# Optimization experiments

Measured on AMD Instinct MI355X. Metric: run time of the kernel, lower is better.

## Reference

```python
import jax, jax.numpy as jnp
import numpy as np

N = 100_000   # nodes
E = 1_600_000 # edges (avg degree 16)
D0, D1, D2 = 128, 64, 64


def _linp(key, n_out, n_in):
    kw, kb = jax.random.split(key)
    s = 1.0 / np.sqrt(n_in)
    W = jax.random.uniform(kw, (n_out, n_in), jnp.float32, -s, s)
    b = jax.random.uniform(kb, (n_out,), jnp.float32, -s, s)
    return W, b


def setup_inputs() -> dict:
    key = jax.random.key(0)
    ks = jax.random.split(key, 9)
    h = jax.random.normal(ks[0], (N, D0), jnp.float32)
    # guarantee every row has at least one edge (avoids empty-row softmax / 0-std NaNs)
    rows = jnp.concatenate([jnp.arange(N, dtype=jnp.int32),
                            jax.random.randint(ks[1], (E - N,), 0, N, jnp.int32)])
    cols = jax.random.randint(ks[2], (E,), 0, N, jnp.int32)
    edge_index = jnp.stack([rows, cols])  # [2, E], row = softmax segment
    W11, b11 = _linp(ks[3], D1, D0)
    W12, b12 = _linp(ks[4], 1, D1)
    W13, b13 = _linp(ks[5], D1, D0)
    W21, b21 = _linp(ks[6], D2, D1)
    W22, b22 = _linp(ks[7], 1, D2)
    W23, b23 = _linp(ks[8], D2, D1)
    return dict(h=h, edge_index=edge_index,
                W11=W11, b11=b11, W12=W12, b12=b12, W13=W13, b13=b13,
                W21=W21, b21=b21, W22=W22, b22=b22, W23=W23, b23=b23)


def reference(h, edge_index, W11, b11, W12, b12, W13, b13,
              W21, b21, W22, b22, W23, b23):
    src, dst = edge_index[0], edge_index[1]

    def gat_layer(x, Wa, ba, We, be, Wv, bv):
        a = jnp.tanh(x @ Wa.T + ba)                       # [N, d] node scores (l11/l21)
        e = jnp.tanh((a[src] + a[dst]) @ We.T + be)[:, 0] # [E] per-edge logit (l12/l22)
        # per-row (segment) softmax over src = row index
        m = jax.ops.segment_max(e, src, num_segments=N)
        ex = jnp.exp(e - m[src])
        denom = jax.ops.segment_sum(ex, src, num_segments=N)
        att = ex / denom[src]                             # [E]
        v = jnp.tanh(x @ Wv.T + bv)                       # [N, d] values (l13/l23)
        out = jax.ops.segment_sum(att[:, None] * v[dst], src, num_segments=N)  # sparse mm
        return out / jnp.std(out, -1, keepdims=True, ddof=1)  # torch.std is unbiased

    h = gat_layer(h, W11, b11, W12, b12, W13, b13)
    h = gat_layer(h, W21, b21, W22, b22, W23, b23)
    return h
```

## Files before the change

### kernel.cpp

```cpp
#include <hip/hip_runtime.h>


#define WS_ALIGN 256
#define BIN_SHIFT 7
#define BIN_NODES 128
#define BIN_CAP 2560
#define MAX_BINS 1024
#define EPB 4096

typedef __attribute__((ext_vector_type(8))) short short8;
typedef __attribute__((ext_vector_type(4))) float f32x4;

__device__ __forceinline__ float wave_sum(float x) {
#pragma unroll
  for (int m = 32; m > 0; m >>= 1) x += __shfl_xor(x, m, 64);
  return x;
}

__device__ __forceinline__ float fast_tanh(float x) {
  x = fminf(15.f, fmaxf(-15.f, x));
  float e = __expf(2.f * x);
  return (e - 1.f) * __builtin_amdgcn_rcpf(e + 1.f);
}

__device__ __forceinline__ void prepw_one(const float* __restrict__ Wa,
                                          const float* __restrict__ Wv,
                                          short* __restrict__ Wh, short* __restrict__ Wl,
                                          int K, int i) {
  int KBLK = K / 32;
  int j = i & 7;
  int c = (i >> 3) & 15;
  int q = (i >> 7) & 3;
  int r = i >> 9;
  int nt = r / KBLK, kb = r - nt * KBLK;
  int row = nt * 16 + c;
  int col = kb * 32 + q * 8 + j;
  float f = (row < 64) ? Wa[row * K + col] : Wv[(row - 64) * K + col];
  unsigned u = __float_as_uint(f);
  float hf = __uint_as_float(u & 0xffff0000u);
  Wh[i] = (short)(u >> 16);
  Wl[i] = (short)(__float_as_uint(f - hf) >> 16);
}

__global__ void k_setup(const float* __restrict__ W11, const float* __restrict__ W13,
                        short* __restrict__ Wh1, short* __restrict__ Wl1,
                        const float* __restrict__ W21, const float* __restrict__ W23,
                        short* __restrict__ Wh2, short* __restrict__ Wl2,
                        int* __restrict__ cursor, int nb) {
  int i = blockIdx.x * 256 + threadIdx.x;
  if (i < 16384) {
    prepw_one(W11, W13, Wh1, Wl1, 128, i);
  } else if (i < 16384 + 8192) {
    prepw_one(W21, W23, Wh2, Wl2, 64, i - 16384);
  } else {
    int b = i - 24576;
    if (b < nb) cursor[b] = b * BIN_CAP;
  }
}

__global__ __launch_bounds__(256) void k_bin(const int* __restrict__ src,
                                             const int* __restrict__ dst,
                                             int* __restrict__ cursor,
                                             int* __restrict__ binned, int E, int nb) {
  __shared__ int ssrc[EPB];
  __shared__ int sdst[EPB];
  __shared__ int hist[MAX_BINS];
  __shared__ int base[MAX_BINS];
  int t = threadIdx.x;
  for (int i = t; i < nb; i += 256) hist[i] = 0;
  __syncthreads();
  int e0 = blockIdx.x * EPB;
  for (int i = t; i < EPB; i += 256) {
    int e = e0 + i;
    int sv = -1, dv = 0;
    if (e < E) {
      sv = src[e];
      dv = dst[e];
      atomicAdd(&hist[sv >> BIN_SHIFT], 1);
    }
    ssrc[i] = sv;
    sdst[i] = dv;
  }
  __syncthreads();
  for (int b = t; b < nb; b += 256) {
    int c = hist[b];
    base[b] = c ? atomicAdd(&cursor[b], c) : 0;
    hist[b] = 0;
  }
  __syncthreads();
  for (int i = t; i < EPB; i += 256) {
    int sv = ssrc[i];
    if (sv >= 0) {
      int b = sv >> BIN_SHIFT;
      int r = atomicAdd(&hist[b], 1);
      int pos = base[b] + r;
      if (pos < (b + 1) * BIN_CAP)
        binned[pos] = (sdst[i] << BIN_SHIFT) | (sv & (BIN_NODES - 1));
    }
  }
}

__global__ __launch_bounds__(256) void k_sort_bin(int* __restrict__ binned,
                                                  const int* __restrict__ cursor,
                                                  int* __restrict__ rs,
                                                  int* __restrict__ re, int n) {
  __shared__ int ents[BIN_CAP];
  __shared__ int sorted[BIN_CAP];
  __shared__ int hist[BIN_NODES];
  __shared__ int scan[BIN_NODES];
  __shared__ int cur[BIN_NODES];
  int bin = blockIdx.x;
  int t = threadIdx.x;
  int nbase = bin << BIN_SHIFT;
  int cnt = cursor[bin] - bin * BIN_CAP;
  if (cnt > BIN_CAP) cnt = BIN_CAP;
  if (t < BIN_NODES) hist[t] = 0;
  __syncthreads();
  int* bp = binned + (size_t)bin * BIN_CAP;
  for (int i = t; i < cnt; i += 256) {
    int pk = bp[i];
    ents[i] = pk;
    atomicAdd(&hist[pk & (BIN_NODES - 1)], 1);
  }
  __syncthreads();
  if (t < BIN_NODES) scan[t] = hist[t];
  __syncthreads();
  for (int off = 1; off < BIN_NODES; off <<= 1) {
    int add = (t < BIN_NODES && t >= off) ? scan[t - off] : 0;
    __syncthreads();
    if (t < BIN_NODES) scan[t] += add;
    __syncthreads();
  }
  if (t < BIN_NODES) {
    int ex = scan[t] - hist[t];
    cur[t] = ex;
    int node = nbase + t;
    if (node < n) {
      rs[node] = bin * BIN_CAP + ex;
      re[node] = bin * BIN_CAP + ex + hist[t];
    }
  }
  __syncthreads();
  for (int i = t; i < cnt; i += 256) {
    int pk = ents[i];
    int pos = atomicAdd(&cur[pk & (BIN_NODES - 1)], 1);
    sorted[pos] = pk;
  }
  __syncthreads();
  for (int i = t; i < cnt; i += 256) {
    int pk = sorted[i];
    int node = pk & (BIN_NODES - 1);
    int hi = scan[node];
    int lo = hi - hist[node];
    int r = lo;
    for (int j = lo; j < hi; j++) {
      int pj = sorted[j];
      r += (pj < pk) || (pj == pk && j < i);
    }
    ents[r] = pk >> BIN_SHIFT;
  }
  __syncthreads();
  for (int i = t; i < cnt; i += 256) bp[i] = ents[i];
}

template <int K>
__global__ __launch_bounds__(256) void k_node(
    const float* __restrict__ x, const short* __restrict__ Wh,
    const short* __restrict__ Wl, const float* __restrict__ ba,
    const float* __restrict__ we, const float* __restrict__ bv,
    float* __restrict__ v_out, float* __restrict__ s_out, int n) {
  constexpr int KBLK = K / 32;
  constexpr int KP = K + 4;
  __shared__ float sx[64 * KP];
  int t = threadIdx.x;
  int l = t & 63;
  int w = t >> 6;
  int q = l >> 4, c = l & 15;
  int node0b = blockIdx.x * 64;

  {
    const float4* xg = (const float4*)(x + (size_t)node0b * K);
    constexpr int R4 = K / 4;
#pragma unroll
    for (int it = 0; it < 64 * R4 / 256; it++) {
      int i = it * 256 + t;
      int r = i / R4, k4 = i - r * R4;
      float4 val = (node0b + r < n) ? xg[i] : (float4){0.f, 0.f, 0.f, 0.f};
      *(float4*)&sx[r * KP + k4 * 4] = val;
    }
  }
  __syncthreads();

  int node0w = node0b + w * 16;
  if (node0w >= n) return;

  const short8* WhF = (const short8*)Wh;
  const short8* WlF = (const short8*)Wl;

  f32x4 acc[8];
#pragma unroll
  for (int i = 0; i < 8; i++) acc[i] = (f32x4){0.f, 0.f, 0.f, 0.f};

  const float* xl = sx + (w * 16 + c) * KP;

#pragma unroll 1
  for (int kb = 0; kb < KBLK; kb++) {
    float4 x0 = *(const float4*)&xl[kb * 32 + q * 8];
    float4 x1 = *(const float4*)&xl[kb * 32 + q * 8 + 4];
    float xv[8] = {x0.x, x0.y, x0.z, x0.w, x1.x, x1.y, x1.z, x1.w};
    short8 ah, al;
#pragma unroll
    for (int j = 0; j < 8; j++) {
      unsigned u = __float_as_uint(xv[j]);
      ah[j] = (short)(u >> 16);
      float hf = __uint_as_float(u & 0xffff0000u);
      al[j] = (short)(__float_as_uint(xv[j] - hf) >> 16);
    }
#pragma unroll
    for (int nt = 0; nt < 8; nt++) {
      short8 wh = WhF[(size_t)(nt * KBLK + kb) * 64 + l];
      short8 wl = WlF[(size_t)(nt * KBLK + kb) * 64 + l];
      acc[nt] = __builtin_amdgcn_mfma_f32_16x16x32_bf16(ah, wh, acc[nt], 0, 0, 0);
      acc[nt] = __builtin_amdgcn_mfma_f32_16x16x32_bf16(ah, wl, acc[nt], 0, 0, 0);
      acc[nt] = __builtin_amdgcn_mfma_f32_16x16x32_bf16(al, wh, acc[nt], 0, 0, 0);
    }
  }

  float p[4] = {0.f, 0.f, 0.f, 0.f};
#pragma unroll
  for (int nt = 0; nt < 4; nt++) {
    int o = nt * 16 + c;
    float bav = ba[o], wev = we[o];
#pragma unroll
    for (int r = 0; r < 4; r++) p[r] += fast_tanh(acc[nt][r] + bav) * wev;
  }
#pragma unroll
  for (int mm = 1; mm < 16; mm <<= 1) {
#pragma unroll
    for (int r = 0; r < 4; r++) p[r] += __shfl_xor(p[r], mm, 64);
  }
  if (c == 0) {
#pragma unroll
    for (int r = 0; r < 4; r++) {
      int node = node0w + q * 4 + r;
      if (node < n) s_out[node] = p[r];
    }
  }
#pragma unroll
  for (int nt = 4; nt < 8; nt++) {
    int o = (nt - 4) * 16 + c;
    float bvv = bv[o];
#pragma unroll
    for (int r = 0; r < 4; r++) {
      int node = node0w + q * 4 + r;
      if (node < n)
        v_out[(size_t)node * 64 + o] = fast_tanh(acc[nt][r] + bvv);
    }
  }
}

__global__ __launch_bounds__(256) void k_aggr(const int* __restrict__ rs,
                                              const int* __restrict__ re,
                                              const int* __restrict__ col,
                                              const float* __restrict__ s,
                                              const float* __restrict__ be_p,
                                              const float* __restrict__ v,
                                              float* __restrict__ out, int n) {
  int gw = (int)((blockIdx.x * 256 + threadIdx.x) >> 6);
  int l = threadIdx.x & 63;
  if (gw >= n) return;
  int e0 = rs[gw], e1 = re[gw];
  float srow = s[gw];
  float be = be_p[0];
  int es = l >> 4;
  int g = l & 15;
  float a0 = 0.f, a1 = 0.f, a2 = 0.f, a3 = 0.f;
  float dl = 0.f;

  for (int base = e0; base < e1; base += 64) {
    int m = e1 - base;
    if (m > 64) m = 64;
    bool act = (l < m);
    int c = 0;
    if (act) c = col[base + l];
    float sc = act ? s[c] : 0.f;
    float w = act ? __expf(fast_tanh(srow + sc + be)) : 0.f;
    dl += w;
    int iters = (m + 7) >> 3;
    for (int it = 0; it < iters; it++) {
      int j0 = (it << 3) + es;
      int c0 = __shfl(c, j0);
      int c1 = __shfl(c, j0 + 4);
      float4 p0 = *(const float4*)(v + ((size_t)c0 << 6) + (g << 2));
      float4 p1 = *(const float4*)(v + ((size_t)c1 << 6) + (g << 2));
      float w0 = __shfl(w, j0);
      float w1 = __shfl(w, j0 + 4);
      a0 = fmaf(w0, p0.x, a0);
      a1 = fmaf(w0, p0.y, a1);
      a2 = fmaf(w0, p0.z, a2);
      a3 = fmaf(w0, p0.w, a3);
      a0 = fmaf(w1, p1.x, a0);
      a1 = fmaf(w1, p1.y, a1);
      a2 = fmaf(w1, p1.z, a2);
      a3 = fmaf(w1, p1.w, a3);
    }
  }

#pragma unroll
  for (int mm = 16; mm < 64; mm <<= 1) {
    a0 += __shfl_xor(a0, mm, 64);
    a1 += __shfl_xor(a1, mm, 64);
    a2 += __shfl_xor(a2, mm, 64);
    a3 += __shfl_xor(a3, mm, 64);
  }
  float denom = wave_sum(dl);
  float inv = __builtin_amdgcn_rcpf(denom);
  float o0 = a0 * inv, o1 = a1 * inv, o2 = a2 * inv, o3 = a3 * inv;
  float t0 = o0 + o1 + o2 + o3;
  float t1 = o0 * o0 + o1 * o1 + o2 * o2 + o3 * o3;
#pragma unroll
  for (int mm = 1; mm < 16; mm <<= 1) {
    t0 += __shfl_xor(t0, mm, 64);
    t1 += __shfl_xor(t1, mm, 64);
  }
  float var = (t1 - t0 * t0 * (1.0f / 64.f)) * (1.0f / 63.f);
  float isd = __builtin_amdgcn_rsqf(var);
  if (es == 0) {
    float4 r = {o0 * isd, o1 * isd, o2 * isd, o3 * isd};
    *(float4*)&out[(size_t)gw * 64 + (g << 2)] = r;
  }
}

extern "C" void kernel_launch(void* const* d_in, const int* in_sizes, int n_in,
                              void* d_out, int out_size, void* d_ws, size_t ws_size,
                              hipStream_t stream) {
  const float* h = (const float*)d_in[0];
  const int* ei = (const int*)d_in[1];
  const float* W11 = (const float*)d_in[2];
  const float* b11 = (const float*)d_in[3];
  const float* W12 = (const float*)d_in[4];
  const float* b12 = (const float*)d_in[5];
  const float* W13 = (const float*)d_in[6];
  const float* b13 = (const float*)d_in[7];
  const float* W21 = (const float*)d_in[8];
  const float* b21 = (const float*)d_in[9];
  const float* W22 = (const float*)d_in[10];
  const float* b22 = (const float*)d_in[11];
  const float* W23 = (const float*)d_in[12];
  const float* b23 = (const float*)d_in[13];

  const int N = in_sizes[0] / 128;
  const int E = in_sizes[1] / 2;
  const int* src = ei;
  const int* dst = ei + E;
  const int NB = (N + BIN_NODES - 1) >> BIN_SHIFT;

  char* p = (char*)d_ws;
  auto alloc = [&](size_t bytes) -> void* {
    void* r = (void*)p;
    p += (bytes + WS_ALIGN - 1) / WS_ALIGN * WS_ALIGN;
    return r;
  };
  int* cursor = (int*)alloc((size_t)NB * 4);
  int* binned = (int*)alloc((size_t)NB * BIN_CAP * 4);
  int* rsb = (int*)alloc((size_t)N * 4);
  int* reb = (int*)alloc((size_t)N * 4);
  float* sbuf = (float*)alloc((size_t)N * 4);
  float* vbuf = (float*)alloc((size_t)N * 64 * 4);
  float* out1 = (float*)alloc((size_t)N * 64 * 4);
  short* Wh1 = (short*)alloc(128 * 128 * 2);
  short* Wl1 = (short*)alloc(128 * 128 * 2);
  short* Wh2 = (short*)alloc(128 * 64 * 2);
  short* Wl2 = (short*)alloc(128 * 64 * 2);

  k_setup<<<(24576 + NB + 255) / 256, 256, 0, stream>>>(
      W11, W13, Wh1, Wl1, W21, W23, Wh2, Wl2, cursor, NB);

  k_bin<<<(E + EPB - 1) / EPB, 256, 0, stream>>>(src, dst, cursor, binned, E, NB);
  k_sort_bin<<<NB, 256, 0, stream>>>(binned, cursor, rsb, reb, N);

  k_node<128><<<(N + 63) / 64, 256, 0, stream>>>(h, Wh1, Wl1, b11, W12, b13, vbuf, sbuf, N);
  k_aggr<<<(N * 64 + 255) / 256, 256, 0, stream>>>(rsb, reb, binned, sbuf, b12, vbuf, out1, N);

  k_node<64><<<(N + 63) / 64, 256, 0, stream>>>(out1, Wh2, Wl2, b21, W22, b23, vbuf, sbuf, N);
  k_aggr<<<(N * 64 + 255) / 256, 256, 0, stream>>>(rsb, reb, binned, sbuf, b22, vbuf, (float*)d_out, N);
}
```

Baseline: 324.9 us.

## Store value features as bf16 and use persistent grid-stride aggregation

```diff
diff --git a/kernel.cpp b/kernel.cpp
--- a/kernel.cpp
+++ b/kernel.cpp
@@ -7,6 +7,7 @@
 #define BIN_CAP 2560
 #define MAX_BINS 1024
 #define EPB 4096
+#define AGGR_BLOCKS 2048
 
 typedef __attribute__((ext_vector_type(8))) short short8;
 typedef __attribute__((ext_vector_type(4))) float f32x4;
@@ -21,6 +22,12 @@
   x = fminf(15.f, fmaxf(-15.f, x));
   float e = __expf(2.f * x);
   return (e - 1.f) * __builtin_amdgcn_rcpf(e + 1.f);
+}
+
+__device__ __forceinline__ unsigned short f32_to_bf16_rne(float f) {
+  unsigned u = __float_as_uint(f);
+  unsigned r = u + 0x7fffu + ((u >> 16) & 1u);
+  return (unsigned short)(r >> 16);
 }
 
 __device__ __forceinline__ void prepw_one(const float* __restrict__ Wa,
@@ -168,7 +175,7 @@
     const float* __restrict__ x, const short* __restrict__ Wh,
     const short* __restrict__ Wl, const float* __restrict__ ba,
     const float* __restrict__ we, const float* __restrict__ bv,
-    float* __restrict__ v_out, float* __restrict__ s_out, int n) {
+    unsigned short* __restrict__ v_out, float* __restrict__ s_out, int n) {
   constexpr int KBLK = K / 32;
   constexpr int KP = K + 4;
   __shared__ float sx[64 * KP];
@@ -254,7 +261,7 @@
     for (int r = 0; r < 4; r++) {
       int node = node0w + q * 4 + r;
       if (node < n)
-        v_out[(size_t)node * 64 + o] = fast_tanh(acc[nt][r] + bvv);
+        v_out[(size_t)node * 64 + o] = f32_to_bf16_rne(fast_tanh(acc[nt][r] + bvv));
     }
   }
 }
@@ -264,70 +271,87 @@
                                               const int* __restrict__ col,
                                               const float* __restrict__ s,
                                               const float* __restrict__ be_p,
-                                              const float* __restrict__ v,
+                                              const unsigned short* __restrict__ v,
                                               float* __restrict__ out, int n) {
-  int gw = (int)((blockIdx.x * 256 + threadIdx.x) >> 6);
+  int wid = (int)((blockIdx.x * 256 + threadIdx.x) >> 6);
+  int nw = AGGR_BLOCKS * 4;
   int l = threadIdx.x & 63;
-  if (gw >= n) return;
-  int e0 = rs[gw], e1 = re[gw];
-  float srow = s[gw];
-  float be = be_p[0];
   int es = l >> 4;
   int g = l & 15;
-  float a0 = 0.f, a1 = 0.f, a2 = 0.f, a3 = 0.f;
-  float dl = 0.f;
-
-  for (int base = e0; base < e1; base += 64) {
-    int m = e1 - base;
-    if (m > 64) m = 64;
-    bool act = (l < m);
-    int c = 0;
-    if (act) c = col[base + l];
-    float sc = act ? s[c] : 0.f;
-    float w = act ? __expf(fast_tanh(srow + sc + be)) : 0.f;
-    dl += w;
-    int iters = (m + 7) >> 3;
-    for (int it = 0; it < iters; it++) {
-      int j0 = (it << 3) + es;
-      int c0 = __shfl(c, j0);
-      int c1 = __shfl(c, j0 + 4);
-      float4 p0 = *(const float4*)(v + ((size_t)c0 << 6) + (g << 2));
-      float4 p1 = *(const float4*)(v + ((size_t)c1 << 6) + (g << 2));
-      float w0 = __shfl(w, j0);
-      float w1 = __shfl(w, j0 + 4);
-      a0 = fmaf(w0, p0.x, a0);
-      a1 = fmaf(w0, p0.y, a1);
-      a2 = fmaf(w0, p0.z, a2);
-      a3 = fmaf(w0, p0.w, a3);
-      a0 = fmaf(w1, p1.x, a0);
-      a1 = fmaf(w1, p1.y, a1);
-      a2 = fmaf(w1, p1.z, a2);
-      a3 = fmaf(w1, p1.w, a3);
-    }
-  }
-
-#pragma unroll
-  for (int mm = 16; mm < 64; mm <<= 1) {
-    a0 += __shfl_xor(a0, mm, 64);
-    a1 += __shfl_xor(a1, mm, 64);
-    a2 += __shfl_xor(a2, mm, 64);
-    a3 += __shfl_xor(a3, mm, 64);
-  }
-  float denom = wave_sum(dl);
-  float inv = __builtin_amdgcn_rcpf(denom);
-  float o0 = a0 * inv, o1 = a1 * inv, o2 = a2 * inv, o3 = a3 * inv;
-  float t0 = o0 + o1 + o2 + o3;
-  float t1 = o0 * o0 + o1 * o1 + o2 * o2 + o3 * o3;
-#pragma unroll
-  for (int mm = 1; mm < 16; mm <<= 1) {
-    t0 += __shfl_xor(t0, mm, 64);
-    t1 += __shfl_xor(t1, mm, 64);
-  }
-  float var = (t1 - t0 * t0 * (1.0f / 64.f)) * (1.0f / 63.f);
-  float isd = __builtin_amdgcn_rsqf(var);
-  if (es == 0) {
-    float4 r = {o0 * isd, o1 * isd, o2 * isd, o3 * isd};
-    *(float4*)&out[(size_t)gw * 64 + (g << 2)] = r;
+  float be = be_p[0];
+
+  for (int gw = wid; gw < n; gw += nw) {
+    int e0 = rs[gw], e1 = re[gw];
+    float srow = s[gw];
+    float a0 = 0.f, a1 = 0.f, a2 = 0.f, a3 = 0.f;
+    float dl = 0.f;
+
+    for (int base = e0; base < e1; base += 64) {
+      int m = e1 - base;
+      if (m > 64) m = 64;
+      bool act = (l < m);
+      int c = act ? col[base + l] : 0;
+      float sc = act ? s[c] : 0.f;
+      float w = act ? __expf(fast_tanh(srow + sc + be)) : 0.f;
+      dl += w;
+      int iters = (m + 15) >> 4;
+      for (int it = 0; it < iters; it++) {
+        int j = (it << 4) + es;
+        int c0 = __shfl(c, j);
+        int c1 = __shfl(c, j + 4);
+        int c2 = __shfl(c, j + 8);
+        int c3 = __shfl(c, j + 12);
+        uint2 p0 = *(const uint2*)(v + ((size_t)c0 << 6) + (g << 2));
+        uint2 p1 = *(const uint2*)(v + ((size_t)c1 << 6) + (g << 2));
+        uint2 p2 = *(const uint2*)(v + ((size_t)c2 << 6) + (g << 2));
+        uint2 p3 = *(const uint2*)(v + ((size_t)c3 << 6) + (g << 2));
+        float w0 = __shfl(w, j);
+        float w1 = __shfl(w, j + 4);
+        float w2 = __shfl(w, j + 8);
+        float w3 = __shfl(w, j + 12);
+        a0 = fmaf(w0, __uint_as_float(p0.x << 16), a0);
+        a1 = fmaf(w0, __uint_as_float(p0.x & 0xffff0000u), a1);
+        a2 = fmaf(w0, __uint_as_float(p0.y << 16), a2);
+        a3 = fmaf(w0, __uint_as_float(p0.y & 0xffff0000u), a3);
+        a0 = fmaf(w1, __uint_as_float(p1.x << 16), a0);
+        a1 = fmaf(w1, __uint_as_float(p1.x & 0xffff0000u), a1);
+        a2 = fmaf(w1, __uint_as_float(p1.y << 16), a2);
+        a3 = fmaf(w1, __uint_as_float(p1.y & 0xffff0000u), a3);
+        a0 = fmaf(w2, __uint_as_float(p2.x << 16), a0);
+        a1 = fmaf(w2, __uint_as_float(p2.x & 0xffff0000u), a1);
+        a2 = fmaf(w2, __uint_as_float(p2.y << 16), a2);
+        a3 = fmaf(w2, __uint_as_float(p2.y & 0xffff0000u), a3);
+        a0 = fmaf(w3, __uint_as_float(p3.x << 16), a0);
+        a1 = fmaf(w3, __uint_as_float(p3.x & 0xffff0000u), a1);
+        a2 = fmaf(w3, __uint_as_float(p3.y << 16), a2);
+        a3 = fmaf(w3, __uint_as_float(p3.y & 0xffff0000u), a3);
+      }
+    }
+
+    float b0 = a0, b1 = a1, b2 = a2, b3 = a3;
+#pragma unroll
+    for (int mm = 16; mm < 64; mm <<= 1) {
+      b0 += __shfl_xor(b0, mm, 64);
+      b1 += __shfl_xor(b1, mm, 64);
+      b2 += __shfl_xor(b2, mm, 64);
+      b3 += __shfl_xor(b3, mm, 64);
+    }
+    float denom = wave_sum(dl);
+    float inv = __builtin_amdgcn_rcpf(denom);
+    float o0 = b0 * inv, o1 = b1 * inv, o2 = b2 * inv, o3 = b3 * inv;
+    float t0 = o0 + o1 + o2 + o3;
+    float t1 = o0 * o0 + o1 * o1 + o2 * o2 + o3 * o3;
+#pragma unroll
+    for (int mm = 1; mm < 16; mm <<= 1) {
+      t0 += __shfl_xor(t0, mm, 64);
+      t1 += __shfl_xor(t1, mm, 64);
+    }
+    float var = (t1 - t0 * t0 * (1.0f / 64.f)) * (1.0f / 63.f);
+    float isd = __builtin_amdgcn_rsqf(var);
+    if (es == 0) {
+      float4 r = {o0 * isd, o1 * isd, o2 * isd, o3 * isd};
+      *(float4*)&out[(size_t)gw * 64 + (g << 2)] = r;
+    }
   }
 }
 
@@ -366,7 +390,7 @@
   int* rsb = (int*)alloc((size_t)N * 4);
   int* reb = (int*)alloc((size_t)N * 4);
   float* sbuf = (float*)alloc((size_t)N * 4);
-  float* vbuf = (float*)alloc((size_t)N * 64 * 4);
+  unsigned short* vbuf = (unsigned short*)alloc((size_t)N * 64 * 2);
   float* out1 = (float*)alloc((size_t)N * 64 * 4);
   short* Wh1 = (short*)alloc(128 * 128 * 2);
   short* Wl1 = (short*)alloc(128 * 128 * 2);
@@ -380,8 +404,8 @@
   k_sort_bin<<<NB, 256, 0, stream>>>(binned, cursor, rsb, reb, N);
 
   k_node<128><<<(N + 63) / 64, 256, 0, stream>>>(h, Wh1, Wl1, b11, W12, b13, vbuf, sbuf, N);
-  k_aggr<<<(N * 64 + 255) / 256, 256, 0, stream>>>(rsb, reb, binned, sbuf, b12, vbuf, out1, N);
+  k_aggr<<<AGGR_BLOCKS, 256, 0, stream>>>(rsb, reb, binned, sbuf, b12, vbuf, out1, N);
 
   k_node<64><<<(N + 63) / 64, 256, 0, stream>>>(out1, Wh2, Wl2, b21, W22, b23, vbuf, sbuf, N);
-  k_aggr<<<(N * 64 + 255) / 256, 256, 0, stream>>>(rsb, reb, binned, sbuf, b22, vbuf, (float*)d_out, N);
-}
+  k_aggr<<<AGGR_BLOCKS, 256, 0, stream>>>(rsb, reb, binned, sbuf, b22, vbuf, (float*)d_out, N);
+}
```

Result: faster. 296.9 us (-8.6%).
